# Kernel optimization log

Measured on AMD Instinct MI355X. Metric: run time of the kernel, lower is better.

## Reference

```python
import jax, jax.numpy as jnp
import numpy as np

D_MODEL = 1024
NUM_HEADS = 16
D_HEAD = D_MODEL // NUM_HEADS
THETA = 10000.0


def _apply_rope(x, pos):
    # x: [B, H, S, Dh]; pos: [S]
    inv_freq = 1.0 / (THETA ** (jnp.arange(0, D_HEAD, 2, dtype=jnp.float32) / D_HEAD))  # [Dh/2]
    freqs = pos[:, None].astype(x.dtype) * inv_freq.astype(x.dtype)  # [S, Dh/2]
    cos = jnp.cos(freqs)  # [S, Dh/2]
    sin = jnp.sin(freqs)
    x1 = x[..., 0::2]  # [B, H, S, Dh/2]
    x2 = x[..., 1::2]
    even = x1 * cos - x2 * sin
    odd = x1 * sin + x2 * cos
    # interleave back: stack on last axis then flatten
    out = jnp.stack([even, odd], axis=-1).reshape(x.shape)
    return out


def setup_inputs() -> dict:
    key = jax.random.key(0)
    k0, k1, k2, k3, k4 = jax.random.split(key, 5)
    B, S = 2, 2048
    scale = 0.02
    return {
        "in_features": jax.random.normal(k0, (B, S, D_MODEL), dtype=jnp.float32),
        "Wq": jax.random.normal(k1, (D_MODEL, D_MODEL), dtype=jnp.float32) * scale,
        "Wk": jax.random.normal(k2, (D_MODEL, D_MODEL), dtype=jnp.float32) * scale,
        "Wv": jax.random.normal(k3, (D_MODEL, D_MODEL), dtype=jnp.float32) * scale,
        "Wo": jax.random.normal(k4, (D_MODEL, D_MODEL), dtype=jnp.float32) * scale,
    }


def reference(in_features, Wq, Wk, Wv, Wo):
    B, S, _ = in_features.shape
    H, Dh = NUM_HEADS, D_HEAD

    def proj(W):
        # torch Linear: y = x @ W^T; split heads -> [B, H, S, Dh]
        y = jnp.einsum('bsd,ed->bse', in_features, W)
        return y.reshape(B, S, H, Dh).transpose(0, 2, 1, 3)

    q = proj(Wq)
    k = proj(Wk)
    v = proj(Wv)

    pos = jnp.arange(S)
    q = _apply_rope(q, pos)
    k = _apply_rope(k, pos)

    scores = jnp.einsum('bhqd,bhkd->bhqk', q, k) / jnp.sqrt(jnp.asarray(Dh, q.dtype))
    causal = jnp.tril(jnp.ones((S, S), dtype=bool))  # True = keep
    scores = jnp.where(causal[None, None, :, :], scores, -jnp.inf)
    att = jax.nn.softmax(scores, axis=-1)
    out = jnp.einsum('bhqk,bhkd->bhqd', att, v)  # [B, H, S, Dh]
    out = out.transpose(0, 2, 1, 3).reshape(B, S, H * Dh)
    return jnp.einsum('bsd,ed->bse', out, Wo)
```

## Files before the change

kernel.cpp:

```cpp
#include <hip/hip_runtime.h>
#include <hip/hip_bf16.h>
#include <math.h>

#define D_MODEL 1024
#define NHEAD 16
#define DHEAD 64
#define SEQ 2048
#define BATCH 2
#define MTOT (BATCH * SEQ)

typedef __attribute__((ext_vector_type(8))) short bf16x8;
typedef __attribute__((ext_vector_type(4))) float f32x4;

static __device__ __forceinline__ ushort f2b(float x) {
  __hip_bfloat16 h = __float2bfloat16(x);
  union { __hip_bfloat16 h; ushort u; } cv; cv.h = h; return cv.u;
}

#define GLLDS16(gp, lp)                                                     \
  __builtin_amdgcn_global_load_lds(                                         \
      (const __attribute__((address_space(1))) unsigned int*)(gp),          \
      (__attribute__((address_space(3))) unsigned int*)(lp), 16, 0, 0)

#define QSCALE 0.18033688011112042f

__global__ __launch_bounds__(256)
void prep(const float* __restrict__ X, const float* __restrict__ Wq,
          const float* __restrict__ Wk, const float* __restrict__ Wv,
          const float* __restrict__ Wo, ushort* __restrict__ Xb,
          ushort* __restrict__ Wqb, ushort* __restrict__ Wkb,
          ushort* __restrict__ Wvb, ushort* __restrict__ Wob,
          float2* __restrict__ tbl) {
  int bid = blockIdx.x;
  if (bid >= 8192) {
    int idx = (bid - 8192) * 256 + threadIdx.x;
    int s = idx >> 5, i = idx & 31;
    float inv = exp2f((float)i * -0.4152410118609203f);
    float sn, cs;
    sincosf((float)s * inv, &sn, &cs);
    tbl[idx] = make_float2(cs, sn);
    return;
  }
  const float* in;
  ushort* out;
  int i;
  if (bid < 4096) {
    in = X; out = Xb; i = bid * 256 + threadIdx.x;
  } else {
    int ws = (bid - 4096) >> 10;
    in = (ws == 0) ? Wq : (ws == 1) ? Wk : (ws == 2) ? Wv : Wo;
    out = (ws == 0) ? Wqb : (ws == 1) ? Wkb : (ws == 2) ? Wvb : Wob;
    i = ((bid - 4096) & 1023) * 256 + threadIdx.x;
  }
  float4 v = ((const float4*)in)[i];
  ushort4 o;
  o.x = f2b(v.x); o.y = f2b(v.y); o.z = f2b(v.z); o.w = f2b(v.w);
  ((ushort4*)out)[i] = o;
}

__global__ __launch_bounds__(256)
void gemm_bf16(const ushort* __restrict__ A,
               const ushort* __restrict__ W0, const ushort* __restrict__ W1,
               const ushort* __restrict__ W2,
               const float2* __restrict__ tbl,
               float* __restrict__ outF,
               ushort* __restrict__ o0, ushort* __restrict__ o1,
               ushort* __restrict__ o2, int mode) {
  __shared__ ushort As[128 * 32];
  __shared__ ushort Bs[128 * 32];
  const int tid = threadIdx.x;
  const int lane = tid & 63;
  const int w = tid >> 6;
  const int quad = lane >> 4, l15 = lane & 15;
  const int wy = w >> 1, wx = w & 1;
  const int m0 = blockIdx.y * 128, n0 = blockIdx.x * 128;
  const int z = blockIdx.z;
  const ushort* W = (z == 0) ? W0 : (z == 1) ? W1 : W2;
  ushort* outB = (z == 0) ? o0 : (z == 1) ? o1 : o2;

  const int r0 = tid >> 2, c0 = tid & 3;
  const int gc = c0 ^ (((r0 >> 2) ^ r0) & 3);
  const ushort* Ag0 = A + (size_t)(m0 + r0) * D_MODEL + gc * 8;
  const ushort* Ag1 = A + (size_t)(m0 + r0 + 64) * D_MODEL + gc * 8;
  const ushort* Wg0 = W + (size_t)(n0 + r0) * D_MODEL + gc * 8;
  const ushort* Wg1 = W + (size_t)(n0 + r0 + 64) * D_MODEL + gc * 8;

  const int sw = (quad ^ (l15 >> 2) ^ l15) & 3;

  f32x4 acc[4][4];
#pragma unroll
  for (int i = 0; i < 4; ++i)
#pragma unroll
    for (int j = 0; j < 4; ++j) acc[i][j] = (f32x4){0.f, 0.f, 0.f, 0.f};

  for (int kt = 0; kt < D_MODEL / 32; ++kt) {
    if (kt) __syncthreads();
    GLLDS16(Ag0 + kt * 32, &As[(size_t)tid * 8]);
    GLLDS16(Ag1 + kt * 32, &As[(size_t)(tid + 256) * 8]);
    GLLDS16(Wg0 + kt * 32, &Bs[(size_t)tid * 8]);
    GLLDS16(Wg1 + kt * 32, &Bs[(size_t)(tid + 256) * 8]);
    __syncthreads();

    bf16x8 af[4], bfr[4];
#pragma unroll
    for (int mt = 0; mt < 4; ++mt) {
      int row = wy * 64 + mt * 16 + l15;
      af[mt] = *(const bf16x8*)&As[(row * 4 + sw) * 8];
    }
#pragma unroll
    for (int nt = 0; nt < 4; ++nt) {
      int row = wx * 64 + nt * 16 + l15;
      bfr[nt] = *(const bf16x8*)&Bs[(row * 4 + sw) * 8];
    }
#pragma unroll
    for (int mt = 0; mt < 4; ++mt)
#pragma unroll
      for (int nt = 0; nt < 4; ++nt)
        acc[mt][nt] = __builtin_amdgcn_mfma_f32_16x16x32_bf16(
            af[mt], bfr[nt], acc[mt][nt], 0, 0, 0);
  }

  const float qsc = (z == 0) ? QSCALE : 1.0f;
#pragma unroll
  for (int mt = 0; mt < 4; ++mt) {
    int m_base = m0 + wy * 64 + mt * 16 + quad * 4;
    int b = m_base >> 11, s_base = m_base & (SEQ - 1);
#pragma unroll
    for (int nt = 0; nt < 4; ++nt) {
      int n = n0 + wx * 64 + nt * 16 + l15;
      if (mode == 0) {
#pragma unroll
        for (int r = 0; r < 4; ++r)
          outF[(size_t)(m_base + r) * D_MODEL + n] = acc[mt][nt][r];
      } else {
        int h = n >> 6, dh = n & 63;
        if (z == 2) {
          ushort4 o;
          o.x = f2b(acc[mt][nt][0]); o.y = f2b(acc[mt][nt][1]);
          o.z = f2b(acc[mt][nt][2]); o.w = f2b(acc[mt][nt][3]);
          *(ushort4*)&outB[((size_t)(b * NHEAD + h) * DHEAD + dh) * SEQ + s_base] = o;
        } else {
          int i = nt * 8 + (l15 >> 1);
          bool evn = !(l15 & 1);
#pragma unroll
          for (int r = 0; r < 4; ++r) {
            float v = acc[mt][nt][r];
            float pv = __shfl_xor(v, 1);
            float2 csn = tbl[(s_base + r) * 32 + i];
            v = v * csn.x + (evn ? -pv * csn.y : pv * csn.y);
            v *= qsc;
            outB[(((size_t)(b * NHEAD + h)) * SEQ + s_base + r) * DHEAD + dh] = f2b(v);
          }
        }
      }
    }
  }
}

__global__ __launch_bounds__(256)
void flash_mfma(const ushort* __restrict__ Q, const ushort* __restrict__ K,
                const ushort* __restrict__ Vt, ushort* __restrict__ O) {
  __shared__ ushort Ks[64 * 64];
  __shared__ ushort Vs[64 * 64];
  __shared__ ushort Ps[4][16][68];
  const int tid = threadIdx.x;
  const int lane = tid & 63, w = tid >> 6;
  const int quad = lane >> 4, l15 = lane & 15;
  const int h = blockIdx.y, b = blockIdx.z;
  const int qt = (h >= 8) ? (31 - blockIdx.x) : blockIdx.x;
  const int bh = b * NHEAD + h;

  const ushort* Qrow = Q + ((size_t)bh * SEQ + qt * 64 + w * 16 + l15) * 64;
  bf16x8 aq0 = *(const bf16x8*)(Qrow + quad * 8);
  bf16x8 aq1 = *(const bf16x8*)(Qrow + 32 + quad * 8);

  const int rl = tid >> 3;
  const int gsc = (tid & 7) ^ (rl & 7);
  const ushort* Kg0 = K + ((size_t)bh * SEQ + rl) * 64 + gsc * 8;
  const ushort* Kg1 = Kg0 + (size_t)32 * 64;
  const ushort* Vg0 = Vt + ((size_t)bh * 64 + rl) * SEQ + gsc * 8;
  const ushort* Vg1 = Vg0 + (size_t)32 * SEQ;

  const int sA = (quad ^ (l15 & 7)) * 8;
  const int sB = sA ^ 32;

  float rsl[4];
  f32x4 accO[4];
#pragma unroll
  for (int r = 0; r < 4; ++r) rsl[r] = 0.f;
#pragma unroll
  for (int nt = 0; nt < 4; ++nt) accO[nt] = (f32x4){0.f, 0.f, 0.f, 0.f};

  float4 pk0 = *(const float4*)(Kg0);
  float4 pk1 = *(const float4*)(Kg1);
  float4 pv0 = *(const float4*)(Vg0);
  float4 pv1 = *(const float4*)(Vg1);

  const int qrow0 = qt * 64 + w * 16 + quad * 4;

  for (int kt = 0; kt <= qt; ++kt) {
    __syncthreads();
    *(float4*)&Ks[tid * 8]        = pk0;
    *(float4*)&Ks[2048 + tid * 8] = pk1;
    *(float4*)&Vs[tid * 8]        = pv0;
    *(float4*)&Vs[2048 + tid * 8] = pv1;
    __syncthreads();
    if (kt < qt) {
      pk0 = *(const float4*)(Kg0 + (size_t)(kt + 1) * 64 * 64);
      pk1 = *(const float4*)(Kg1 + (size_t)(kt + 1) * 64 * 64);
      pv0 = *(const float4*)(Vg0 + (kt + 1) * 64);
      pv1 = *(const float4*)(Vg1 + (kt + 1) * 64);
    }

    f32x4 sc[4];
#pragma unroll
    for (int nt = 0; nt < 4; ++nt) {
      const ushort* kr = &Ks[(nt * 16 + l15) * 64];
      bf16x8 bk0 = *(const bf16x8*)(kr + sA);
      bf16x8 bk1 = *(const bf16x8*)(kr + sB);
      f32x4 zz = (f32x4){0.f, 0.f, 0.f, 0.f};
      zz = __builtin_amdgcn_mfma_f32_16x16x32_bf16(aq0, bk0, zz, 0, 0, 0);
      zz = __builtin_amdgcn_mfma_f32_16x16x32_bf16(aq1, bk1, zz, 0, 0, 0);
      sc[nt] = zz;
    }

    const bool diag = (kt == qt);
#pragma unroll
    for (int nt = 0; nt < 4; ++nt) {
      int kg = kt * 64 + nt * 16 + l15;
#pragma unroll
      for (int r = 0; r < 4; ++r) {
        float p = __builtin_amdgcn_exp2f(sc[nt][r]);
        if (diag && kg > qrow0 + r) p = 0.f;
        Ps[w][quad * 4 + r][nt * 16 + l15] = f2b(p);
        rsl[r] += p;
      }
    }

    bf16x8 ap0 = *(const bf16x8*)&Ps[w][l15][quad * 8];
    bf16x8 ap1 = *(const bf16x8*)&Ps[w][l15][32 + quad * 8];
#pragma unroll
    for (int nt = 0; nt < 4; ++nt) {
      const ushort* vr = &Vs[(nt * 16 + l15) * 64];
      bf16x8 bv0 = *(const bf16x8*)(vr + sA);
      bf16x8 bv1 = *(const bf16x8*)(vr + sB);
      accO[nt] = __builtin_amdgcn_mfma_f32_16x16x32_bf16(ap0, bv0, accO[nt], 0, 0, 0);
      accO[nt] = __builtin_amdgcn_mfma_f32_16x16x32_bf16(ap1, bv1, accO[nt], 0, 0, 0);
    }
  }

#pragma unroll
  for (int r = 0; r < 4; ++r) {
#pragma unroll
    for (int off = 1; off < 16; off <<= 1) rsl[r] += __shfl_xor(rsl[r], off);
  }

#pragma unroll
  for (int r = 0; r < 4; ++r) {
    float invl = 1.f / rsl[r];
    int qrow = qt * 64 + w * 16 + quad * 4 + r;
    size_t base = ((size_t)(b * SEQ + qrow)) * D_MODEL + h * 64;
#pragma unroll
    for (int nt = 0; nt < 4; ++nt)
      O[base + nt * 16 + l15] = f2b(accO[nt][r] * invl);
  }
}

extern "C" void kernel_launch(void* const* d_in, const int* in_sizes, int n_in,
                              void* d_out, int out_size, void* d_ws, size_t ws_size,
                              hipStream_t stream) {
  const float* X  = (const float*)d_in[0];
  const float* Wq = (const float*)d_in[1];
  const float* Wk = (const float*)d_in[2];
  const float* Wv = (const float*)d_in[3];
  const float* Wo = (const float*)d_in[4];
  float* out = (float*)d_out;

  ushort* Xb  = (ushort*)d_ws;
  ushort* Wqb = Xb  + (size_t)MTOT * D_MODEL;
  ushort* Wkb = Wqb + (size_t)D_MODEL * D_MODEL;
  ushort* Wvb = Wkb + (size_t)D_MODEL * D_MODEL;
  ushort* Wob = Wvb + (size_t)D_MODEL * D_MODEL;
  ushort* Qw  = Wob + (size_t)D_MODEL * D_MODEL;
  ushort* Kw  = Qw  + (size_t)MTOT * D_MODEL;
  ushort* Vtw = Kw  + (size_t)MTOT * D_MODEL;
  ushort* At  = Vtw + (size_t)MTOT * D_MODEL;
  float2* tbl = (float2*)(At + (size_t)MTOT * D_MODEL);

  prep<<<8448, 256, 0, stream>>>(X, Wq, Wk, Wv, Wo, Xb, Wqb, Wkb, Wvb, Wob, tbl);

  gemm_bf16<<<dim3(D_MODEL / 128, MTOT / 128, 3), 256, 0, stream>>>(
      Xb, Wqb, Wkb, Wvb, tbl, nullptr, Qw, Kw, Vtw, 1);

  flash_mfma<<<dim3(SEQ / 64, NHEAD, BATCH), 256, 0, stream>>>(Qw, Kw, Vtw, At);

  gemm_bf16<<<dim3(D_MODEL / 128, MTOT / 128, 1), 256, 0, stream>>>(
      At, Wob, nullptr, nullptr, tbl, out, nullptr, nullptr, nullptr, 0);
}
```

Baseline: 180.0 us.

## Keep softmax probabilities in registers by transposing flash attention MFMAs

Swaps the MFMA operand order so the score tile comes out transposed, letting each lane hold probabilities for one query row along the key dimension. Those values are packed directly into the B operand of the PV MFMA, which removes the LDS staging buffer for P and its write/read round trip. To match the register layout expected by the PV MFMA, the V projection epilogue writes V^T with a permuted sequence order inside each 32-wide group. Row sums now need only two cross-lane shuffles, and the output store becomes a vectorized 4-wide write. The cost is a tighter coupling between the projection kernel's V layout and the attention kernel, which must stay consistent for correctness.

```diff
diff --git a/kernel.cpp b/kernel.cpp
--- a/kernel.cpp
+++ b/kernel.cpp
@@ -135,10 +135,12 @@
       } else {
         int h = n >> 6, dh = n & 63;
         if (z == 2) {
+          int p_base = (s_base & ~31) | (((s_base >> 2) & 3) << 3) |
+                       (((s_base >> 4) & 1) << 2);
           ushort4 o;
           o.x = f2b(acc[mt][nt][0]); o.y = f2b(acc[mt][nt][1]);
           o.z = f2b(acc[mt][nt][2]); o.w = f2b(acc[mt][nt][3]);
-          *(ushort4*)&outB[((size_t)(b * NHEAD + h) * DHEAD + dh) * SEQ + s_base] = o;
+          *(ushort4*)&outB[((size_t)(b * NHEAD + h) * DHEAD + dh) * SEQ + p_base] = o;
         } else {
           int i = nt * 8 + (l15 >> 1);
           bool evn = !(l15 & 1);
@@ -162,7 +164,6 @@
                 const ushort* __restrict__ Vt, ushort* __restrict__ O) {
   __shared__ ushort Ks[64 * 64];
   __shared__ ushort Vs[64 * 64];
-  __shared__ ushort Ps[4][16][68];
   const int tid = threadIdx.x;
   const int lane = tid & 63, w = tid >> 6;
   const int quad = lane >> 4, l15 = lane & 15;
@@ -170,7 +171,8 @@
   const int qt = (h >= 8) ? (31 - blockIdx.x) : blockIdx.x;
   const int bh = b * NHEAD + h;
 
-  const ushort* Qrow = Q + ((size_t)bh * SEQ + qt * 64 + w * 16 + l15) * 64;
+  const int qrow = qt * 64 + w * 16 + l15;
+  const ushort* Qrow = Q + ((size_t)bh * SEQ + qrow) * 64;
   bf16x8 aq0 = *(const bf16x8*)(Qrow + quad * 8);
   bf16x8 aq1 = *(const bf16x8*)(Qrow + 32 + quad * 8);
 
@@ -184,10 +186,8 @@
   const int sA = (quad ^ (l15 & 7)) * 8;
   const int sB = sA ^ 32;
 
-  float rsl[4];
+  float rsl = 0.f;
   f32x4 accO[4];
-#pragma unroll
-  for (int r = 0; r < 4; ++r) rsl[r] = 0.f;
 #pragma unroll
   for (int nt = 0; nt < 4; ++nt) accO[nt] = (f32x4){0.f, 0.f, 0.f, 0.f};
 
@@ -195,8 +195,6 @@
   float4 pk1 = *(const float4*)(Kg1);
   float4 pv0 = *(const float4*)(Vg0);
   float4 pv1 = *(const float4*)(Vg1);
-
-  const int qrow0 = qt * 64 + w * 16 + quad * 4;
 
   for (int kt = 0; kt <= qt; ++kt) {
     __syncthreads();
@@ -219,50 +217,54 @@
       bf16x8 bk0 = *(const bf16x8*)(kr + sA);
       bf16x8 bk1 = *(const bf16x8*)(kr + sB);
       f32x4 zz = (f32x4){0.f, 0.f, 0.f, 0.f};
-      zz = __builtin_amdgcn_mfma_f32_16x16x32_bf16(aq0, bk0, zz, 0, 0, 0);
-      zz = __builtin_amdgcn_mfma_f32_16x16x32_bf16(aq1, bk1, zz, 0, 0, 0);
+      zz = __builtin_amdgcn_mfma_f32_16x16x32_bf16(bk0, aq0, zz, 0, 0, 0);
+      zz = __builtin_amdgcn_mfma_f32_16x16x32_bf16(bk1, aq1, zz, 0, 0, 0);
       sc[nt] = zz;
     }
 
     const bool diag = (kt == qt);
-#pragma unroll
-    for (int nt = 0; nt < 4; ++nt) {
-      int kg = kt * 64 + nt * 16 + l15;
+    uint pk[8];
+#pragma unroll
+    for (int nt = 0; nt < 4; ++nt) {
+      int kbase = kt * 64 + nt * 16 + quad * 4;
+      ushort us[4];
 #pragma unroll
       for (int r = 0; r < 4; ++r) {
         float p = __builtin_amdgcn_exp2f(sc[nt][r]);
-        if (diag && kg > qrow0 + r) p = 0.f;
-        Ps[w][quad * 4 + r][nt * 16 + l15] = f2b(p);
-        rsl[r] += p;
+        if (diag && kbase + r > qrow) p = 0.f;
+        rsl += p;
+        us[r] = f2b(p);
       }
-    }
-
-    bf16x8 ap0 = *(const bf16x8*)&Ps[w][l15][quad * 8];
-    bf16x8 ap1 = *(const bf16x8*)&Ps[w][l15][32 + quad * 8];
+      pk[nt * 2]     = (uint)us[0] | ((uint)us[1] << 16);
+      pk[nt * 2 + 1] = (uint)us[2] | ((uint)us[3] << 16);
+    }
+    union { uint u[4]; bf16x8 v; } B0, B1;
+    B0.u[0] = pk[0]; B0.u[1] = pk[1]; B0.u[2] = pk[2]; B0.u[3] = pk[3];
+    B1.u[0] = pk[4]; B1.u[1] = pk[5]; B1.u[2] = pk[6]; B1.u[3] = pk[7];
+
 #pragma unroll
     for (int nt = 0; nt < 4; ++nt) {
       const ushort* vr = &Vs[(nt * 16 + l15) * 64];
-      bf16x8 bv0 = *(const bf16x8*)(vr + sA);
-      bf16x8 bv1 = *(const bf16x8*)(vr + sB);
-      accO[nt] = __builtin_amdgcn_mfma_f32_16x16x32_bf16(ap0, bv0, accO[nt], 0, 0, 0);
-      accO[nt] = __builtin_amdgcn_mfma_f32_16x16x32_bf16(ap1, bv1, accO[nt], 0, 0, 0);
-    }
-  }
-
-#pragma unroll
-  for (int r = 0; r < 4; ++r) {
-#pragma unroll
-    for (int off = 1; off < 16; off <<= 1) rsl[r] += __shfl_xor(rsl[r], off);
-  }
-
-#pragma unroll
-  for (int r = 0; r < 4; ++r) {
-    float invl = 1.f / rsl[r];
-    int qrow = qt * 64 + w * 16 + quad * 4 + r;
-    size_t base = ((size_t)(b * SEQ + qrow)) * D_MODEL + h * 64;
-#pragma unroll
-    for (int nt = 0; nt < 4; ++nt)
-      O[base + nt * 16 + l15] = f2b(accO[nt][r] * invl);
+      bf16x8 av0 = *(const bf16x8*)(vr + sA);
+      bf16x8 av1 = *(const bf16x8*)(vr + sB);
+      accO[nt] = __builtin_amdgcn_mfma_f32_16x16x32_bf16(av0, B0.v, accO[nt], 0, 0, 0);
+      accO[nt] = __builtin_amdgcn_mfma_f32_16x16x32_bf16(av1, B1.v, accO[nt], 0, 0, 0);
+    }
+  }
+
+  rsl += __shfl_xor(rsl, 16);
+  rsl += __shfl_xor(rsl, 32);
+  float invl = 1.f / rsl;
+
+  size_t base = ((size_t)(b * SEQ + qrow)) * D_MODEL + h * 64;
+#pragma unroll
+  for (int nt = 0; nt < 4; ++nt) {
+    ushort4 o;
+    o.x = f2b(accO[nt][0] * invl);
+    o.y = f2b(accO[nt][1] * invl);
+    o.z = f2b(accO[nt][2] * invl);
+    o.w = f2b(accO[nt][3] * invl);
+    *(ushort4*)&O[base + nt * 16 + quad * 4] = o;
   }
 }
 
```

Result: faster. 176.2 us (median of 2 runs) (-2.1%).

## Compute transposed S tile in registers, permute V layout, split keys across warps

Applied to the files above, without the earlier changes.

The flash attention kernel now computes S^T = K·Q^T, so the exponentiated probabilities land in registers in exactly the operand layout the PV MFMA needs. This removes the LDS round trip through the Ps buffer. To make that work, the V projection store permutes the sequence index within each 32-element group. The four warps now split as two query groups times two key halves, and the key-half partial outputs and row sums are combined through shared memory at the end. Launch bounds are also raised to request four blocks per CU, which adds an epilogue reduction and register pressure in exchange for less LDS traffic.

```diff
diff --git a/kernel.cpp b/kernel.cpp
--- a/kernel.cpp
+++ b/kernel.cpp
@@ -135,10 +135,12 @@
       } else {
         int h = n >> 6, dh = n & 63;
         if (z == 2) {
+          int p_base = (s_base & ~31) | (((s_base >> 2) & 3) << 3) |
+                       (((s_base >> 4) & 1) << 2);
           ushort4 o;
           o.x = f2b(acc[mt][nt][0]); o.y = f2b(acc[mt][nt][1]);
           o.z = f2b(acc[mt][nt][2]); o.w = f2b(acc[mt][nt][3]);
-          *(ushort4*)&outB[((size_t)(b * NHEAD + h) * DHEAD + dh) * SEQ + s_base] = o;
+          *(ushort4*)&outB[((size_t)(b * NHEAD + h) * DHEAD + dh) * SEQ + p_base] = o;
         } else {
           int i = nt * 8 + (l15 >> 1);
           bool evn = !(l15 & 1);
@@ -157,22 +159,29 @@
   }
 }
 
-__global__ __launch_bounds__(256)
+__global__ __launch_bounds__(256, 4)
 void flash_mfma(const ushort* __restrict__ Q, const ushort* __restrict__ K,
                 const ushort* __restrict__ Vt, ushort* __restrict__ O) {
-  __shared__ ushort Ks[64 * 64];
-  __shared__ ushort Vs[64 * 64];
-  __shared__ ushort Ps[4][16][68];
+  __shared__ ushort KVs[2 * 64 * 64];
+  __shared__ float RSr[2][2][16];
+  ushort* Ks = KVs;
+  ushort* Vs = KVs + 4096;
   const int tid = threadIdx.x;
   const int lane = tid & 63, w = tid >> 6;
   const int quad = lane >> 4, l15 = lane & 15;
+  const int i = w & 1, j = w >> 1;
   const int h = blockIdx.y, b = blockIdx.z;
   const int qt = (h >= 8) ? (31 - blockIdx.x) : blockIdx.x;
   const int bh = b * NHEAD + h;
 
-  const ushort* Qrow = Q + ((size_t)bh * SEQ + qt * 64 + w * 16 + l15) * 64;
-  bf16x8 aq0 = *(const bf16x8*)(Qrow + quad * 8);
-  bf16x8 aq1 = *(const bf16x8*)(Qrow + 32 + quad * 8);
+  const int qbase = qt * 64 + j * 32;
+  const ushort* Qr0 = Q + ((size_t)bh * SEQ + qbase + l15) * 64;
+  const ushort* Qr1 = Qr0 + 16 * 64;
+  bf16x8 aq[2][2];
+  aq[0][0] = *(const bf16x8*)(Qr0 + quad * 8);
+  aq[0][1] = *(const bf16x8*)(Qr0 + 32 + quad * 8);
+  aq[1][0] = *(const bf16x8*)(Qr1 + quad * 8);
+  aq[1][1] = *(const bf16x8*)(Qr1 + 32 + quad * 8);
 
   const int rl = tid >> 3;
   const int gsc = (tid & 7) ^ (rl & 7);
@@ -181,22 +190,22 @@
   const ushort* Vg0 = Vt + ((size_t)bh * 64 + rl) * SEQ + gsc * 8;
   const ushort* Vg1 = Vg0 + (size_t)32 * SEQ;
 
-  const int sA = (quad ^ (l15 & 7)) * 8;
+  const int x7 = l15 & 7;
+  const int sA = (quad ^ x7) * 8;
   const int sB = sA ^ 32;
-
-  float rsl[4];
-  f32x4 accO[4];
-#pragma unroll
-  for (int r = 0; r < 4; ++r) rsl[r] = 0.f;
-#pragma unroll
-  for (int nt = 0; nt < 4; ++nt) accO[nt] = (f32x4){0.f, 0.f, 0.f, 0.f};
+  const int sV = ((i * 4 + quad) ^ x7) * 8;
+
+  float rsl[2] = {0.f, 0.f};
+  f32x4 accO[4][2];
+#pragma unroll
+  for (int d = 0; d < 4; ++d)
+#pragma unroll
+    for (int g = 0; g < 2; ++g) accO[d][g] = (f32x4){0.f, 0.f, 0.f, 0.f};
 
   float4 pk0 = *(const float4*)(Kg0);
   float4 pk1 = *(const float4*)(Kg1);
   float4 pv0 = *(const float4*)(Vg0);
   float4 pv1 = *(const float4*)(Vg1);
-
-  const int qrow0 = qt * 64 + w * 16 + quad * 4;
 
   for (int kt = 0; kt <= qt; ++kt) {
     __syncthreads();
@@ -206,63 +215,96 @@
     *(float4*)&Vs[2048 + tid * 8] = pv1;
     __syncthreads();
     if (kt < qt) {
-      pk0 = *(const float4*)(Kg0 + (size_t)(kt + 1) * 64 * 64);
-      pk1 = *(const float4*)(Kg1 + (size_t)(kt + 1) * 64 * 64);
+      pk0 = *(const float4*)(Kg0 + (size_t)(kt + 1) * 4096);
+      pk1 = *(const float4*)(Kg1 + (size_t)(kt + 1) * 4096);
       pv0 = *(const float4*)(Vg0 + (kt + 1) * 64);
       pv1 = *(const float4*)(Vg1 + (kt + 1) * 64);
     }
 
-    f32x4 sc[4];
-#pragma unroll
-    for (int nt = 0; nt < 4; ++nt) {
-      const ushort* kr = &Ks[(nt * 16 + l15) * 64];
+    f32x4 sc[2][2];
+#pragma unroll
+    for (int mt = 0; mt < 2; ++mt) {
+      const ushort* kr = &Ks[(i * 32 + mt * 16 + l15) * 64];
       bf16x8 bk0 = *(const bf16x8*)(kr + sA);
       bf16x8 bk1 = *(const bf16x8*)(kr + sB);
-      f32x4 zz = (f32x4){0.f, 0.f, 0.f, 0.f};
-      zz = __builtin_amdgcn_mfma_f32_16x16x32_bf16(aq0, bk0, zz, 0, 0, 0);
-      zz = __builtin_amdgcn_mfma_f32_16x16x32_bf16(aq1, bk1, zz, 0, 0, 0);
-      sc[nt] = zz;
+#pragma unroll
+      for (int g = 0; g < 2; ++g) {
+        f32x4 zz = (f32x4){0.f, 0.f, 0.f, 0.f};
+        zz = __builtin_amdgcn_mfma_f32_16x16x32_bf16(bk0, aq[g][0], zz, 0, 0, 0);
+        zz = __builtin_amdgcn_mfma_f32_16x16x32_bf16(bk1, aq[g][1], zz, 0, 0, 0);
+        sc[mt][g] = zz;
+      }
     }
 
     const bool diag = (kt == qt);
-#pragma unroll
-    for (int nt = 0; nt < 4; ++nt) {
-      int kg = kt * 64 + nt * 16 + l15;
-#pragma unroll
-      for (int r = 0; r < 4; ++r) {
-        float p = __builtin_amdgcn_exp2f(sc[nt][r]);
-        if (diag && kg > qrow0 + r) p = 0.f;
-        Ps[w][quad * 4 + r][nt * 16 + l15] = f2b(p);
-        rsl[r] += p;
+    uint pb[2][4];
+#pragma unroll
+    for (int mt = 0; mt < 2; ++mt) {
+      int kb = kt * 64 + i * 32 + mt * 16 + quad * 4;
+#pragma unroll
+      for (int g = 0; g < 2; ++g) {
+        int qr = qbase + g * 16 + l15;
+        ushort us[4];
+#pragma unroll
+        for (int r = 0; r < 4; ++r) {
+          float p = __builtin_amdgcn_exp2f(sc[mt][g][r]);
+          if (diag && kb + r > qr) p = 0.f;
+          rsl[g] += p;
+          us[r] = f2b(p);
+        }
+        pb[g][mt * 2]     = (uint)us[0] | ((uint)us[1] << 16);
+        pb[g][mt * 2 + 1] = (uint)us[2] | ((uint)us[3] << 16);
       }
     }
-
-    bf16x8 ap0 = *(const bf16x8*)&Ps[w][l15][quad * 8];
-    bf16x8 ap1 = *(const bf16x8*)&Ps[w][l15][32 + quad * 8];
-#pragma unroll
-    for (int nt = 0; nt < 4; ++nt) {
-      const ushort* vr = &Vs[(nt * 16 + l15) * 64];
-      bf16x8 bv0 = *(const bf16x8*)(vr + sA);
-      bf16x8 bv1 = *(const bf16x8*)(vr + sB);
-      accO[nt] = __builtin_amdgcn_mfma_f32_16x16x32_bf16(ap0, bv0, accO[nt], 0, 0, 0);
-      accO[nt] = __builtin_amdgcn_mfma_f32_16x16x32_bf16(ap1, bv1, accO[nt], 0, 0, 0);
-    }
-  }
-
-#pragma unroll
-  for (int r = 0; r < 4; ++r) {
-#pragma unroll
-    for (int off = 1; off < 16; off <<= 1) rsl[r] += __shfl_xor(rsl[r], off);
-  }
-
-#pragma unroll
-  for (int r = 0; r < 4; ++r) {
-    float invl = 1.f / rsl[r];
-    int qrow = qt * 64 + w * 16 + quad * 4 + r;
-    size_t base = ((size_t)(b * SEQ + qrow)) * D_MODEL + h * 64;
-#pragma unroll
-    for (int nt = 0; nt < 4; ++nt)
-      O[base + nt * 16 + l15] = f2b(accO[nt][r] * invl);
+    union { uint u[4]; bf16x8 v; } P0, P1;
+    P0.u[0] = pb[0][0]; P0.u[1] = pb[0][1]; P0.u[2] = pb[0][2]; P0.u[3] = pb[0][3];
+    P1.u[0] = pb[1][0]; P1.u[1] = pb[1][1]; P1.u[2] = pb[1][2]; P1.u[3] = pb[1][3];
+
+#pragma unroll
+    for (int d = 0; d < 4; ++d) {
+      bf16x8 av = *(const bf16x8*)&Vs[(d * 16 + l15) * 64 + sV];
+      accO[d][0] = __builtin_amdgcn_mfma_f32_16x16x32_bf16(av, P0.v, accO[d][0], 0, 0, 0);
+      accO[d][1] = __builtin_amdgcn_mfma_f32_16x16x32_bf16(av, P1.v, accO[d][1], 0, 0, 0);
+    }
+  }
+
+#pragma unroll
+  for (int g = 0; g < 2; ++g) {
+    rsl[g] += __shfl_xor(rsl[g], 16);
+    rsl[g] += __shfl_xor(rsl[g], 32);
+  }
+
+  __syncthreads();
+  float4* Red = (float4*)KVs;
+  if (i == 1) {
+#pragma unroll
+    for (int d = 0; d < 4; ++d)
+#pragma unroll
+      for (int g = 0; g < 2; ++g)
+        Red[(size_t)j * 512 + (d * 2 + g) * 64 + lane] =
+            (float4){accO[d][g][0], accO[d][g][1], accO[d][g][2], accO[d][g][3]};
+    if (quad == 0) { RSr[j][0][l15] = rsl[0]; RSr[j][1][l15] = rsl[1]; }
+  }
+  __syncthreads();
+  if (i == 0) {
+    float invl[2];
+#pragma unroll
+    for (int g = 0; g < 2; ++g) invl[g] = 1.f / (rsl[g] + RSr[j][g][l15]);
+#pragma unroll
+    for (int d = 0; d < 4; ++d) {
+#pragma unroll
+      for (int g = 0; g < 2; ++g) {
+        float4 o = Red[(size_t)j * 512 + (d * 2 + g) * 64 + lane];
+        int qrow = qbase + g * 16 + l15;
+        size_t base = ((size_t)(b * SEQ + qrow)) * D_MODEL + h * 64 + d * 16 + quad * 4;
+        ushort4 s;
+        s.x = f2b((accO[d][g][0] + o.x) * invl[g]);
+        s.y = f2b((accO[d][g][1] + o.y) * invl[g]);
+        s.z = f2b((accO[d][g][2] + o.z) * invl[g]);
+        s.w = f2b((accO[d][g][3] + o.w) * invl[g]);
+        *(ushort4*)&O[base] = s;
+      }
+    }
   }
 }
 
```

Result: no change. 178.3 us (-1.0%).
